# Performance work log

Measured on AMD Instinct MI355X. Metric: run time of the kernel, lower is better.

## Reference

```python
import jax, jax.numpy as jnp
import numpy as np

# dims
A, T, K, H, NH, F, L = 64, 50, 6, 128, 8, 60, 512
M = A * T * K          # 19200 mode nodes (layout: agent, time, mode)
AT = A * T             # 3200 agent-timestep nodes
NL = 10                # GA layers: t2m,l2m,m2m_h,m2m_a,m2m_s,t2n,l2n,n2n_h,n2n_a,n2n_s
FF = 4 * H
E = 150000


def _ln(x, g, b):
    mu = x.mean(-1, keepdims=True)
    var = jnp.mean((x - mu) ** 2, axis=-1, keepdims=True)
    return (x - mu) * jax.lax.rsqrt(var + 1e-5) * g + b


def _mlp(x, W1, b1, W2, b2):
    return jax.nn.relu(x @ W1 + b1) @ W2 + b2


def _edge_emb(attr, i, eW1, eb1, eW2, eb2):
    # pad raw edge features to width 5 so all embed MLPs share a stacked param layout
    x = jnp.pad(attr, ((0, 0), (0, 5 - attr.shape[-1])))
    return jax.nn.relu(x @ eW1[i] + eb1[i]) @ eW2[i] + eb2[i]


def _segment_softmax(scores, dst, n):
    smax = jax.ops.segment_max(scores, dst, num_segments=n)
    smax = jnp.where(jnp.isfinite(smax), smax, 0.0)
    ex = jnp.exp(scores - smax[dst])
    den = jax.ops.segment_sum(ex, dst, num_segments=n)
    return ex / (den[dst] + 1e-9)


def _graph_attention(i, x_src, x_dst, ei, edge_emb, p):
    (Wq, Wk, Wv, Wo, Wke, Wve, g1, b1, g2, b2, fW1, fb1, fW2, fb2) = p
    src, dst = ei[0], ei[1]
    dh = H // NH
    n_dst = x_dst.shape[0]
    xd = _ln(x_dst, g1[i], b1[i])
    xs = _ln(x_src, g1[i], b1[i])
    q = (xd @ Wq[i]).reshape(n_dst, NH, dh)
    k = (xs @ Wk[i])[src]            # gather per-edge keys  [E,H]
    v = (xs @ Wv[i])[src]
    if edge_emb is not None:
        k = k + edge_emb @ Wke[i]
        v = v + edge_emb @ Wve[i]
    k = k.reshape(-1, NH, dh)
    v = v.reshape(-1, NH, dh)
    scores = jnp.sum(q[dst] * k, axis=-1) / np.sqrt(dh)   # [E,NH]
    attn = _segment_softmax(scores, dst, n_dst)
    agg = jax.ops.segment_sum(attn[..., None] * v, dst, num_segments=n_dst)
    x = x_dst + agg.reshape(n_dst, H) @ Wo[i]
    h = _ln(x, g2[i], b2[i])
    return x + _mlp(h, fW1[i], fb1[i], fW2[i], fb2[i])


def _forward(a_input, l_embs, mode_tokens,
             emb_W1, emb_b1, emb_W2, emb_b2,
             ga_Wq, ga_Wk, ga_Wv, ga_Wo, ga_Wke, ga_Wve,
             ga_g1, ga_b1, ga_g2, ga_b2, ga_fW1, ga_fb1, ga_fW2, ga_fb2,
             tp_W1, tp_b1, tp_W2, tp_b2,
             pa_W1, pa_b1, pa_W2, pa_b2,
             tr_W1, tr_b1, tr_W2, tr_b2,
             t2m_attr, l2m_attr, m2m_h_attr, m2m_a_attr,
             t2m_ei, l2m_ei, m2m_h_ei, m2m_a_ei, m2m_s_ei):
    ga = (ga_Wq, ga_Wk, ga_Wv, ga_Wo, ga_Wke, ga_Wve,
          ga_g1, ga_b1, ga_g2, ga_b2, ga_fW1, ga_fb1, ga_fW2, ga_fb2)
    # agent embedding: TwoLayerMLP on [vel_len, vel_theta, length, width, type]
    a_embs = (jax.nn.relu(a_input @ emb_W1[0] + emb_b1[0]) @ emb_W2[0] + emb_b2[0]).reshape(AT, H)
    # mode tokens broadcast over (agent, time)
    m = jnp.broadcast_to(mode_tokens, (A, T, K, H)).reshape(M, H)
    # edge-attr embeddings (gather-compute pattern)
    t2m_e = _edge_emb(t2m_attr, 1, emb_W1, emb_b1, emb_W2, emb_b2)
    l2m_e = _edge_emb(l2m_attr, 2, emb_W1, emb_b1, emb_W2, emb_b2)
    m2m_h_e = _edge_emb(m2m_h_attr, 3, emb_W1, emb_b1, emb_W2, emb_b2)
    m2m_a_e = _edge_emb(m2m_a_attr, 4, emb_W1, emb_b1, emb_W2, emb_b2)
    # proposal stage
    m = _graph_attention(0, a_embs, m, t2m_ei, t2m_e, ga)
    m = _graph_attention(1, l_embs, m, l2m_ei, l2m_e, ga)
    m = _graph_attention(2, m, m, m2m_h_ei, m2m_h_e, ga)
    m = _graph_attention(3, m, m, m2m_a_ei, m2m_a_e, ga)
    m = _graph_attention(4, m, m, m2m_s_ei, None, ga)
    m_last = m.reshape(A, T, K, H)[:, -1]                 # [A,K,H]
    proposal = _mlp(m_last, tp_W1, tp_b1, tp_W2, tp_b2)   # [A,K,2F]
    anchor = _mlp(proposal, pa_W1, pa_b1, pa_W2, pa_b2)   # [A,K,H]
    # refinement stage on anchor-conditioned mode nodes
    n = (m.reshape(A, T, K, H) + anchor[:, None]).reshape(M, H)
    n = _graph_attention(5, a_embs, n, t2m_ei, t2m_e, ga)
    n = _graph_attention(6, l_embs, n, l2m_ei, l2m_e, ga)
    n = _graph_attention(7, n, n, m2m_h_ei, m2m_h_e, ga)
    n = _graph_attention(8, n, n, m2m_a_ei, m2m_a_e, ga)
    n = _graph_attention(9, n, n, m2m_s_ei, None, ga)
    n_last = n.reshape(A, T, K, H)[:, -1]
    refine = proposal + _mlp(n_last, tr_W1, tr_b1, tr_W2, tr_b2)
    return jnp.stack([proposal, refine])                  # [2,A,K,2F]


def setup_inputs() -> dict:
    key = jax.random.key(0)
    ks = list(jax.random.split(key, 64))
    it = iter(ks)
    nx = lambda: next(it)
    p = lambda *s: 0.02 * jax.random.normal(nx(), s, dtype=jnp.float32)
    inp = {}
    inp['a_input'] = jax.random.normal(nx(), (A, T, 5), dtype=jnp.float32)
    inp['l_embs'] = jax.random.normal(nx(), (L, H), dtype=jnp.float32)
    inp['mode_tokens'] = p(K, H)
    # stacked edge/feature embed MLPs: 0:a,1:t2m,2:l2m,3:m2m_h,4:m2m_a
    inp['emb_W1'] = p(5, 5, H); inp['emb_b1'] = jnp.zeros((5, H), jnp.float32)
    inp['emb_W2'] = p(5, H, H); inp['emb_b2'] = jnp.zeros((5, H), jnp.float32)
    # stacked GraphAttention params
    for nm in ['ga_Wq', 'ga_Wk', 'ga_Wv', 'ga_Wo', 'ga_Wke', 'ga_Wve']:
        inp[nm] = p(NL, H, H)
    inp['ga_g1'] = jnp.ones((NL, H), jnp.float32); inp['ga_b1'] = jnp.zeros((NL, H), jnp.float32)
    inp['ga_g2'] = jnp.ones((NL, H), jnp.float32); inp['ga_b2'] = jnp.zeros((NL, H), jnp.float32)
    inp['ga_fW1'] = p(NL, H, FF); inp['ga_fb1'] = jnp.zeros((NL, FF), jnp.float32)
    inp['ga_fW2'] = p(NL, FF, H); inp['ga_fb2'] = jnp.zeros((NL, H), jnp.float32)
    # heads
    inp['tp_W1'] = p(H, H); inp['tp_b1'] = jnp.zeros((H,), jnp.float32)
    inp['tp_W2'] = p(H, 2 * F); inp['tp_b2'] = jnp.zeros((2 * F,), jnp.float32)
    inp['pa_W1'] = p(2 * F, H); inp['pa_b1'] = jnp.zeros((H,), jnp.float32)
    inp['pa_W2'] = p(H, H); inp['pa_b2'] = jnp.zeros((H,), jnp.float32)
    inp['tr_W1'] = p(H, H); inp['tr_b1'] = jnp.zeros((H,), jnp.float32)
    inp['tr_W2'] = p(H, 2 * F); inp['tr_b2'] = jnp.zeros((2 * F,), jnp.float32)
    # raw edge features
    inp['t2m_attr'] = jax.random.normal(nx(), (E, 4), dtype=jnp.float32)
    inp['l2m_attr'] = jax.random.normal(nx(), (E, 3), dtype=jnp.float32)
    inp['m2m_h_attr'] = jax.random.normal(nx(), (E, 4), dtype=jnp.float32)
    inp['m2m_a_attr'] = jax.random.normal(nx(), (E, 3), dtype=jnp.float32)
    # edge indices (src row range differs per graph)
    ri = lambda hi: jax.random.randint(nx(), (E,), 0, hi, dtype=jnp.int32)
    inp['t2m_ei'] = jnp.stack([ri(AT), ri(M)])
    inp['l2m_ei'] = jnp.stack([ri(L), ri(M)])
    inp['m2m_h_ei'] = jnp.stack([ri(M), ri(M)])
    inp['m2m_a_ei'] = jnp.stack([ri(M), ri(M)])
    inp['m2m_s_ei'] = jnp.stack([ri(M), ri(M)])
    return inp


def reference(a_input, l_embs, mode_tokens,
              emb_W1, emb_b1, emb_W2, emb_b2,
              ga_Wq, ga_Wk, ga_Wv, ga_Wo, ga_Wke, ga_Wve,
              ga_g1, ga_b1, ga_g2, ga_b2, ga_fW1, ga_fb1, ga_fW2, ga_fb2,
              tp_W1, tp_b1, tp_W2, tp_b2,
              pa_W1, pa_b1, pa_W2, pa_b2,
              tr_W1, tr_b1, tr_W2, tr_b2,
              t2m_attr, l2m_attr, m2m_h_attr, m2m_a_attr,
              t2m_ei, l2m_ei, m2m_h_ei, m2m_a_ei, m2m_s_ei):
    return _forward(a_input, l_embs, mode_tokens,
                    emb_W1, emb_b1, emb_W2, emb_b2,
                    ga_Wq, ga_Wk, ga_Wv, ga_Wo, ga_Wke, ga_Wve,
                    ga_g1, ga_b1, ga_g2, ga_b2, ga_fW1, ga_fb1, ga_fW2, ga_fb2,
                    tp_W1, tp_b1, tp_W2, tp_b2,
                    pa_W1, pa_b1, pa_W2, pa_b2,
                    tr_W1, tr_b1, tr_W2, tr_b2,
                    t2m_attr, l2m_attr, m2m_h_attr, m2m_a_attr,
                    t2m_ei, l2m_ei, m2m_h_ei, m2m_a_ei, m2m_s_ei)
```

## Files before the change

### kernel.cpp

```cpp
#include <hip/hip_runtime.h>
#include <hip/hip_bf16.h>
#include <math.h>

#define DEV __device__ __forceinline__

typedef __attribute__((ext_vector_type(4))) float floatx4;
typedef __attribute__((ext_vector_type(8))) __bf16 bf16x8;

static constexpr int A_ = 64, T_ = 50, K_ = 6, H_ = 128, NH_ = 8, F_ = 60, L_ = 512;
static constexpr int M_  = A_ * T_ * K_;
static constexpr int AT_ = A_ * T_;
static constexpr int FF_ = 4 * H_;
static constexpr int NL_ = 10;
static constexpr int P2F = 2 * F_;
static constexpr int AK_ = A_ * K_;
static constexpr size_t WLAY = 196608;

DEV ushort f2bh(float f) {
    unsigned u = __float_as_uint(f);
    unsigned r = u + 0x7FFFu + ((u >> 16) & 1u);
    return (ushort)(r >> 16);
}
DEV float bh2f(ushort h) { return __uint_as_float(((unsigned)h) << 16); }

__global__ __launch_bounds__(256) void ln_kernel(const float* __restrict__ x,
                                                 const float* __restrict__ g,
                                                 const float* __restrict__ b,
                                                 float* __restrict__ y, int n) {
    int row = blockIdx.x * 4 + (threadIdx.x >> 6);
    int lane = threadIdx.x & 63;
    if (row >= n) return;
    const float* xr = x + (size_t)row * H_;
    float v0 = xr[lane], v1 = xr[lane + 64];
    float s = v0 + v1;
    for (int m = 32; m >= 1; m >>= 1) s += __shfl_xor(s, m, 64);
    float mu = s * (1.f / 128.f);
    float d0 = v0 - mu, d1 = v1 - mu;
    float vs = d0 * d0 + d1 * d1;
    for (int m = 32; m >= 1; m >>= 1) vs += __shfl_xor(vs, m, 64);
    float rs = rsqrtf(vs * (1.f / 128.f) + 1e-5f);
    float* yr = y + (size_t)row * H_;
    yr[lane]      = d0 * rs * g[lane] + b[lane];
    yr[lane + 64] = d1 * rs * g[lane + 64] + b[lane + 64];
}

template <int ACT, bool RES, bool OBF>
__global__ __launch_bounds__(256) void mgemm(const float* __restrict__ X,
                                             const ushort* __restrict__ Wh,
                                             const ushort* __restrict__ Wl,
                                             const float* __restrict__ bias,
                                             const float* __restrict__ res,
                                             float* __restrict__ Y,
                                             ushort* __restrict__ Yb,
                                             int n, int Kd, int C) {
    __shared__ ushort lds[4 * 8192];
    ushort* Xh  = lds;
    ushort* Xl  = lds + 8192;
    ushort* Wsh = lds + 16384;
    ushort* Wsl = lds + 24576;
    int row0 = blockIdx.x * 128, col0 = blockIdx.y * 128;
    int tid = threadIdx.x;
    int lane = tid & 63, wid = tid >> 6;
    int rbase = (wid >> 1) * 64, cbase = (wid & 1) * 64;
    int lrow = lane & 15, lk = lane >> 4;
    floatx4 acc[4][4];
#pragma unroll
    for (int a = 0; a < 4; a++)
#pragma unroll
        for (int b2 = 0; b2 < 4; b2++) acc[a][b2] = floatx4{0.f, 0.f, 0.f, 0.f};

    for (int k0 = 0; k0 < Kd; k0 += 64) {
#pragma unroll
        for (int i = 0; i < 8; i++) {
            int idx = tid + i * 256;
            int r = idx >> 4, kc = idx & 15;
            float4 v = *(const float4*)(X + (size_t)(row0 + r) * Kd + k0 + kc * 4);
            ushort h0 = f2bh(v.x), h1 = f2bh(v.y), h2 = f2bh(v.z), h3 = f2bh(v.w);
            ushort l0 = f2bh(v.x - bh2f(h0)), l1 = f2bh(v.y - bh2f(h1)),
                   l2 = f2bh(v.z - bh2f(h2)), l3 = f2bh(v.w - bh2f(h3));
            int base = (r << 6) + (((kc >> 1) ^ (r & 7)) << 3) + ((kc & 1) << 2);
            *(ushort4*)(Xh + base) = make_ushort4(h0, h1, h2, h3);
            *(ushort4*)(Xl + base) = make_ushort4(l0, l1, l2, l3);
        }
#pragma unroll
        for (int i = 0; i < 4; i++) {
            int idx = tid + i * 256;
            int c = idx >> 3, ch = idx & 7;
            int base = (c << 6) + ((ch ^ (c & 7)) << 3);
            size_t go = (size_t)(col0 + c) * Kd + k0 + ch * 8;
            *(float4*)(Wsh + base) = *(const float4*)(Wh + go);
            *(float4*)(Wsl + base) = *(const float4*)(Wl + go);
        }
        __syncthreads();
#pragma unroll
        for (int kk = 0; kk < 2; kk++) {
            int ch = kk * 4 + lk;
            bf16x8 xh[4], xl[4], wh[4], wl[4];
#pragma unroll
            for (int s = 0; s < 4; s++) {
                int r = rbase + s * 16 + lrow;
                int xoff = (r << 6) + ((ch ^ (r & 7)) << 3);
                xh[s] = *(const bf16x8*)(Xh + xoff);
                xl[s] = *(const bf16x8*)(Xl + xoff);
                int c = cbase + s * 16 + lrow;
                int woff = (c << 6) + ((ch ^ (c & 7)) << 3);
                wh[s] = *(const bf16x8*)(Wsh + woff);
                wl[s] = *(const bf16x8*)(Wsl + woff);
            }
#pragma unroll
            for (int sr = 0; sr < 4; sr++)
#pragma unroll
                for (int sc = 0; sc < 4; sc++) {
                    acc[sr][sc] = __builtin_amdgcn_mfma_f32_16x16x32_bf16(wh[sc], xh[sr], acc[sr][sc], 0, 0, 0);
                    acc[sr][sc] = __builtin_amdgcn_mfma_f32_16x16x32_bf16(wl[sc], xh[sr], acc[sr][sc], 0, 0, 0);
                    acc[sr][sc] = __builtin_amdgcn_mfma_f32_16x16x32_bf16(wh[sc], xl[sr], acc[sr][sc], 0, 0, 0);
                }
        }
        __syncthreads();
    }
#pragma unroll
    for (int sr = 0; sr < 4; sr++) {
        int row = row0 + rbase + sr * 16 + lrow;
#pragma unroll
        for (int sc = 0; sc < 4; sc++) {
            int col = col0 + cbase + sc * 16 + lk * 4;
            size_t o = (size_t)row * C + col;
            float4 v = make_float4(acc[sr][sc][0], acc[sr][sc][1],
                                   acc[sr][sc][2], acc[sr][sc][3]);
            if (bias) { float4 bv = *(const float4*)(bias + col);
                        v.x += bv.x; v.y += bv.y; v.z += bv.z; v.w += bv.w; }
            if (ACT == 1) { v.x = fmaxf(v.x, 0.f); v.y = fmaxf(v.y, 0.f);
                            v.z = fmaxf(v.z, 0.f); v.w = fmaxf(v.w, 0.f); }
            if (OBF) {
                *(ushort4*)(Yb + o) = make_ushort4(f2bh(v.x), f2bh(v.y), f2bh(v.z), f2bh(v.w));
            } else {
                if (RES) { float4 rv = *(const float4*)(res + o);
                           v.x += rv.x; v.y += rv.y; v.z += rv.z; v.w += rv.w; }
                *(float4*)(Y + o) = v;
            }
        }
    }
}

__global__ __launch_bounds__(256) void prep_w(const float* __restrict__ Wq,
                                              const float* __restrict__ Wk,
                                              const float* __restrict__ Wv,
                                              const float* __restrict__ Wo,
                                              const float* __restrict__ fW1,
                                              const float* __restrict__ fW2,
                                              ushort* __restrict__ oh,
                                              ushort* __restrict__ ol) {
    int l = blockIdx.y, t = blockIdx.x;
    const float* src; int K, C, tiles_c; size_t obase;
    if (t < 64) {
        int mi = t >> 4; t &= 15;
        src = (mi == 0 ? Wq : mi == 1 ? Wk : mi == 2 ? Wv : Wo) + (size_t)l * 16384;
        K = 128; C = 128; tiles_c = 4; obase = (size_t)l * WLAY + (size_t)mi * 16384;
    } else if (t < 128) {
        t -= 64; src = fW1 + (size_t)l * 65536;
        K = 128; C = 512; tiles_c = 16; obase = (size_t)l * WLAY + 65536;
    } else {
        t -= 128; src = fW2 + (size_t)l * 65536;
        K = 512; C = 128; tiles_c = 4; obase = (size_t)l * WLAY + 131072;
    }
    int tc = t % tiles_c, tk = t / tiles_c;
    __shared__ float tile[32][33];
    int tx = threadIdx.x & 31, ty = threadIdx.x >> 5;
#pragma unroll
    for (int i = 0; i < 4; i++) {
        int k = tk * 32 + ty + i * 8;
        tile[ty + i * 8][tx] = src[(size_t)k * C + tc * 32 + tx];
    }
    __syncthreads();
#pragma unroll
    for (int i = 0; i < 4; i++) {
        int c = tc * 32 + ty + i * 8;
        float v = tile[tx][ty + i * 8];
        ushort h = f2bh(v);
        ushort lo = f2bh(v - bh2f(h));
        size_t o = obase + (size_t)c * K + tk * 32 + tx;
        oh[o] = h; ol[o] = lo;
    }
}

template <int ACT, bool RES>
__global__ void small_gemm(const float* __restrict__ X, const float* __restrict__ W,
                           const float* __restrict__ bias, const float* __restrict__ res,
                           float* __restrict__ Y, int n, int Kd, int C) {
    int idx = blockIdx.x * 256 + threadIdx.x;
    if (idx >= n * C) return;
    int row = idx / C, c = idx - row * C;
    float a = bias ? bias[c] : 0.f;
    const float* xr = X + (size_t)row * Kd;
    for (int k = 0; k < Kd; k++) a = fmaf(xr[k], W[(size_t)k * C + c], a);
    if (ACT == 1) a = fmaxf(a, 0.f);
    if (RES) a += res[idx];
    Y[idx] = a;
}

__global__ __launch_bounds__(256) void combine_fast(const float* __restrict__ eW2,
                                                    const float* __restrict__ Wke,
                                                    const float* __restrict__ Wve,
                                                    float* __restrict__ cW) {
    __shared__ float Xs[128 * 36];
    __shared__ float Ws[32 * 128];
    int x = blockIdx.x;
    int li = x & 7, kv = x >> 3;
    int l = li < 4 ? li : li + 1;
    int g = (li & 3) + 1;
    const float* E2 = eW2 + (size_t)g * 16384;
    const float* Wp = (kv ? Wve : Wke) + (size_t)l * 16384;
    float* out = cW + (size_t)l * 32768 + kv * 128;
    int tid = threadIdx.x;
    int tc = tid & 15, tr = tid >> 4;
    int cA = tc * 4, rA = tr * 4;
    float acc[8][8] = {};
    for (int j0 = 0; j0 < 128; j0 += 32) {
#pragma unroll
        for (int i = 0; i < 4; i++) {
            int idx = tid + i * 256;
            int r = idx >> 3, jc = idx & 7;
            *(float4*)(Xs + r * 36 + jc * 4) =
                *(const float4*)(E2 + (size_t)r * 128 + j0 + jc * 4);
        }
#pragma unroll
        for (int i = 0; i < 4; i++) {
            int idx = tid + i * 256;
            int cc = idx & 31, jj = idx >> 5;
            *(float4*)(Ws + jj * 128 + cc * 4) =
                *(const float4*)(Wp + (size_t)(j0 + jj) * 128 + cc * 4);
        }
        __syncthreads();
#pragma unroll 8
        for (int jj = 0; jj < 32; jj++) {
            float4 w0 = *(const float4*)(Ws + jj * 128 + cA);
            float4 w1 = *(const float4*)(Ws + jj * 128 + cA + 64);
            float xr[8];
#pragma unroll
            for (int i2 = 0; i2 < 4; i2++) {
                xr[i2]     = Xs[(rA + i2) * 36 + jj];
                xr[4 + i2] = Xs[(rA + i2 + 64) * 36 + jj];
            }
#pragma unroll
            for (int i2 = 0; i2 < 8; i2++) {
                float xv = xr[i2];
                acc[i2][0] = fmaf(xv, w0.x, acc[i2][0]);
                acc[i2][1] = fmaf(xv, w0.y, acc[i2][1]);
                acc[i2][2] = fmaf(xv, w0.z, acc[i2][2]);
                acc[i2][3] = fmaf(xv, w0.w, acc[i2][3]);
                acc[i2][4] = fmaf(xv, w1.x, acc[i2][4]);
                acc[i2][5] = fmaf(xv, w1.y, acc[i2][5]);
                acc[i2][6] = fmaf(xv, w1.z, acc[i2][6]);
                acc[i2][7] = fmaf(xv, w1.w, acc[i2][7]);
            }
        }
        __syncthreads();
    }
#pragma unroll
    for (int i = 0; i < 8; i++) {
        int r = (i < 4) ? (rA + i) : (rA + i + 60);
#pragma unroll
        for (int chh = 0; chh < 2; chh++) {
            int c = cA + chh * 64;
            *(float4*)(out + (size_t)r * 256 + c) =
                make_float4(acc[i][chh * 4 + 0], acc[i][chh * 4 + 1],
                            acc[i][chh * 4 + 2], acc[i][chh * 4 + 3]);
        }
    }
}
__global__ void combine_bias(const float* __restrict__ eb2,
                             const float* __restrict__ Wke,
                             const float* __restrict__ Wve,
                             float* __restrict__ cb) {
    int x = blockIdx.x;
    int li = x & 7, kv = x >> 3;
    int l = li < 4 ? li : li + 1;
    int g = (li & 3) + 1;
    const float* Wp = (kv ? Wve : Wke) + (size_t)l * 16384;
    const float* eb = eb2 + g * 128;
    int cc = threadIdx.x;
    float a = 0.f;
    for (int j = 0; j < 128; j++) a = fmaf(eb[j], Wp[(size_t)j * 128 + cc], a);
    cb[l * 256 + kv * 128 + cc] = a;
}

__global__ void zero_i32(int* __restrict__ p, int n) {
    int i = blockIdx.x * 256 + threadIdx.x;
    if (i < n) p[i] = 0;
}
__global__ void hist_kernel(const int* __restrict__ dst, int E, int* __restrict__ deg) {
    int e = blockIdx.x * 256 + threadIdx.x;
    if (e < E) atomicAdd(&deg[dst[e]], 1);
}
__global__ __launch_bounds__(256) void exscan5(const int* __restrict__ deg0,
                                               int* __restrict__ off0,
                                               int* __restrict__ cursor0, int n) {
    int g = blockIdx.x;
    const int* deg = deg0 + (size_t)g * n;
    int* off = off0 + (size_t)g * (n + 1);
    int* cursor = cursor0 + (size_t)g * n;
    __shared__ int wsum[4];
    __shared__ int carry;
    int tid = threadIdx.x, lane = tid & 63, w = tid >> 6;
    if (tid == 0) carry = 0;
    __syncthreads();
    for (int base = 0; base < n; base += 256) {
        int v = (base + tid < n) ? deg[base + tid] : 0;
        int incl = v;
        for (int d = 1; d < 64; d <<= 1) {
            int t = __shfl_up(incl, d, 64);
            if (lane >= d) incl += t;
        }
        if (lane == 63) wsum[w] = incl;
        __syncthreads();
        int woff = 0;
        for (int i = 0; i < w; i++) woff += wsum[i];
        int total = wsum[0] + wsum[1] + wsum[2] + wsum[3];
        int excl = carry + woff + incl - v;
        if (base + tid < n) { off[base + tid] = excl; cursor[base + tid] = excl; }
        __syncthreads();
        if (tid == 0) carry += total;
        __syncthreads();
    }
    if (threadIdx.x == 0) off[n] = carry;
}
__global__ void scatter_kernel(const int* __restrict__ dst, int E,
                               int* __restrict__ cursor, int* __restrict__ eids) {
    int e = blockIdx.x * 256 + threadIdx.x;
    if (e < E) { int p = atomicAdd(&cursor[dst[e]], 1); eids[p] = e; }
}
__global__ void sort_edges(const int* __restrict__ eid, const int* __restrict__ srcArr,
                           const float* __restrict__ attr, int aw, int E,
                           int* __restrict__ esrc, float4* __restrict__ eattr) {
    int pos = blockIdx.x * 256 + threadIdx.x;
    if (pos >= E) return;
    int e = eid[pos];
    esrc[pos] = srcArr[e];
    if (attr) {
        float4 v;
        v.x = attr[(size_t)e * aw + 0];
        v.y = attr[(size_t)e * aw + 1];
        v.z = (aw > 2) ? attr[(size_t)e * aw + 2] : 0.f;
        v.w = (aw > 3) ? attr[(size_t)e * aw + 3] : 0.f;
        eattr[pos] = v;
    }
}

__global__ __launch_bounds__(256) void prep_g(const float* __restrict__ q,
                                              const float* __restrict__ cWl,
                                              const float* __restrict__ cbl,
                                              ushort* __restrict__ g,
                                              float* __restrict__ sb) {
    __shared__ float qs[8 * 132];
    int tid = threadIdx.x;
    int cp = tid & 127, hb = (tid >> 7) * 4;
    float ck[64];
    {
        const float* csrc = cWl + (size_t)cp * 256 + hb * 16;
#pragma unroll
        for (int t4 = 0; t4 < 16; t4++) {
            float4 v = *(const float4*)(csrc + t4 * 4);
            ck[t4 * 4 + 0] = v.x; ck[t4 * 4 + 1] = v.y;
            ck[t4 * 4 + 2] = v.z; ck[t4 * 4 + 3] = v.w;
        }
    }
    int d0 = blockIdx.x * 8;
    {
        int dl = tid >> 5, col = (tid & 31) * 4;
        *(float4*)(qs + dl * 132 + col) = *(const float4*)(q + (size_t)(d0 + dl) * 128 + col);
    }
    __syncthreads();
#pragma unroll
    for (int dl = 0; dl < 8; dl++) {
        const float* qr = qs + dl * 132 + hb * 16;
        float a0 = 0.f, a1 = 0.f, a2 = 0.f, a3 = 0.f;
#pragma unroll
        for (int t = 0; t < 16; t++) {
            a0 = fmaf(ck[t],      qr[t],      a0);
            a1 = fmaf(ck[16 + t], qr[16 + t], a1);
            a2 = fmaf(ck[32 + t], qr[32 + t], a2);
            a3 = fmaf(ck[48 + t], qr[48 + t], a3);
        }
        ushort4 o = make_ushort4(f2bh(a0 * 0.25f), f2bh(a1 * 0.25f),
                                 f2bh(a2 * 0.25f), f2bh(a3 * 0.25f));
        *(ushort4*)(g + (size_t)(d0 + dl) * 1024 + cp * 8 + hb) = o;
    }
    if (tid < 64) {
        int dl = tid >> 3, h = tid & 7;
        const float* qr = qs + dl * 132 + h * 16;
        const float* cbr = cbl + h * 16;
        float a = 0.f;
#pragma unroll
        for (int t = 0; t < 16; t++) a = fmaf(cbr[t], qr[t], a);
        sb[(d0 + dl) * 8 + h] = a * 0.25f;
    }
}

__global__ __launch_bounds__(256) void attn_fact(const int* __restrict__ off,
                                                 const int* __restrict__ esrc,
                                                 const float4* __restrict__ eattr,
                                                 const ushort* __restrict__ g,
                                                 const float* __restrict__ sb,
                                                 const float* __restrict__ eW1,
                                                 const float* __restrict__ eb1,
                                                 const float* __restrict__ q,
                                                 const ushort* __restrict__ kvp,
                                                 ushort* __restrict__ hsum,
                                                 float* __restrict__ vxacc,
                                                 float* __restrict__ den) {
    __shared__ float lds[4 * 144];
    int w = threadIdx.x >> 6, l = threadIdx.x & 63;
    int i = l & 15, hlo = l >> 4;
    float* hw = lds + w * 144;
    int d = blockIdx.x * 4 + w;
    int beg = off[d], end = off[d + 1];
    float q0 = q[(size_t)d * 128 + l] * 0.25f;
    float q1 = q[(size_t)d * 128 + 64 + l] * 0.25f;
    float gA[8], gB[8];
#pragma unroll
    for (int j = 0; j < 8; j++) {
        gA[j] = bh2f(g[(size_t)d * 1024 + (j * 16 + i) * 8 + hlo]);
        gB[j] = bh2f(g[(size_t)d * 1024 + (j * 16 + i) * 8 + hlo + 4]);
    }
    float sbA = sb[d * 8 + hlo], sbB = sb[d * 8 + 4 + hlo];
    float w1a[4], w1b[4];
#pragma unroll
    for (int j = 0; j < 4; j++) { w1a[j] = eW1[j * 128 + l]; w1b[j] = eW1[j * 128 + 64 + l]; }
    float ebA = eb1[l], ebB = eb1[64 + l];
    float dnA = 0.f, dnB = 0.f;
    float accL[8] = {}, accH[8] = {};
    float va0 = 0.f, va1 = 0.f;
    float4 atA = make_float4(0.f, 0.f, 0.f, 0.f), atB = atA;
    ushort kA0 = 0, kA1 = 0, vA0 = 0, vA1 = 0;
    ushort kB0 = 0, kB1 = 0, vB0 = 0, vB1 = 0;
    auto LOADE = [&](int p, float4& at, ushort& ka, ushort& kb, ushort& va, ushort& vb) {
        int s = esrc[p]; at = eattr[p];
        const ushort* r = kvp + (size_t)s * 256;
        ka = r[l]; kb = r[64 + l];
        va = r[128 + l]; vb = r[192 + l];
    };
    if (beg < end) LOADE(beg, atA, kA0, kA1, vA0, vA1);
    if (beg + 1 < end) LOADE(beg + 1, atB, kB0, kB1, vB0, vB1);
    for (int pos = beg; pos < end; pos++) {
        float4 at = atA;
        ushort rk0 = kA0, rk1 = kA1, rv0 = vA0, rv1 = vA1;
        atA = atB; kA0 = kB0; kA1 = kB1; vA0 = vB0; vA1 = vB1;
        if (pos + 2 < end) LOADE(pos + 2, atB, kB0, kB1, vB0, vB1);
        float h0 = fmaxf(ebA + at.x * w1a[0] + at.y * w1a[1] + at.z * w1a[2] + at.w * w1a[3], 0.f);
        float h1 = fmaxf(ebB + at.x * w1b[0] + at.y * w1b[1] + at.z * w1b[2] + at.w * w1b[3], 0.f);
        hw[l] = h0; hw[64 + l] = h1;
        __builtin_amdgcn_wave_barrier();
        float pA = q0 * bh2f(rk0), pB = q1 * bh2f(rk1);
#pragma unroll
        for (int j = 0; j < 8; j++) {
            float hv = hw[j * 16 + i];
            pA = fmaf(hv, gA[j], pA);
            pB = fmaf(hv, gB[j], pB);
        }
#pragma unroll
        for (int msk = 1; msk < 16; msk <<= 1) {
            pA += __shfl_xor(pA, msk, 64);
            pB += __shfl_xor(pB, msk, 64);
        }
        float wA = __expf(pA + sbA);
        float wB = __expf(pB + sbB);
        dnA += wA; dnB += wB;
        va0 = fmaf(wA, bh2f(rv0), va0);
        va1 = fmaf(wB, bh2f(rv1), va1);
        if (i == 0) { hw[128 + hlo] = wA; hw[132 + hlo] = wB; }
        __builtin_amdgcn_wave_barrier();
        float4 WA = *(float4*)(hw + 128), WB = *(float4*)(hw + 132);
#pragma unroll
        for (int j = 0; j < 4; j++) {
            float wa = ((const float*)&WA)[j];
            float wb = ((const float*)&WB)[j];
            accL[j]     = fmaf(wa, h0, accL[j]);
            accH[j]     = fmaf(wa, h1, accH[j]);
            accL[4 + j] = fmaf(wb, h0, accL[4 + j]);
            accH[4 + j] = fmaf(wb, h1, accH[4 + j]);
        }
    }
#pragma unroll
    for (int h = 0; h < 8; h++) {
        hsum[(size_t)d * 1024 + h * 128 + l]      = f2bh(accL[h]);
        hsum[(size_t)d * 1024 + h * 128 + 64 + l] = f2bh(accH[h]);
    }
    vxacc[(size_t)d * 128 + l] = va0;
    vxacc[(size_t)d * 128 + 64 + l] = va1;
    if (i == 0) { den[d * 8 + hlo] = dnA; den[d * 8 + 4 + hlo] = dnB; }
}

__global__ __launch_bounds__(256) void attn_plain(const int* __restrict__ off,
                                                  const int* __restrict__ esrc,
                                                  const float* __restrict__ q,
                                                  const ushort* __restrict__ kvp,
                                                  float* __restrict__ agg) {
    int lane = threadIdx.x & 63;
    int d = blockIdx.x * 4 + (threadIdx.x >> 6);
    int beg = off[d], end = off[d + 1];
    float q0 = q[(size_t)d * 128 + lane] * 0.25f;
    float q1 = q[(size_t)d * 128 + 64 + lane] * 0.25f;
    float den0 = 0.f, den1 = 0.f, acc0 = 0.f, acc1 = 0.f;
    ushort kA0 = 0, kA1 = 0, vA0 = 0, vA1 = 0;
    ushort kB0 = 0, kB1 = 0, vB0 = 0, vB1 = 0;
    auto LOADE = [&](int p, ushort& ka, ushort& kb, ushort& va, ushort& vb) {
        int s = esrc[p];
        const ushort* r = kvp + (size_t)s * 256;
        ka = r[lane]; kb = r[64 + lane];
        va = r[128 + lane]; vb = r[192 + lane];
    };
    if (beg < end) LOADE(beg, kA0, kA1, vA0, vA1);
    if (beg + 1 < end) LOADE(beg + 1, kB0, kB1, vB0, vB1);
    for (int pos = beg; pos < end; pos++) {
        ushort rk0 = kA0, rk1 = kA1, rv0 = vA0, rv1 = vA1;
        kA0 = kB0; kA1 = kB1; vA0 = vB0; vA1 = vB1;
        if (pos + 2 < end) LOADE(pos + 2, kB0, kB1, vB0, vB1);
        float p0 = q0 * bh2f(rk0), p1 = q1 * bh2f(rk1);
#pragma unroll
        for (int msk = 1; msk < 16; msk <<= 1) {
            p0 += __shfl_xor(p0, msk, 64);
            p1 += __shfl_xor(p1, msk, 64);
        }
        float w0 = __expf(p0), w1 = __expf(p1);
        den0 += w0; den1 += w1;
        acc0 = fmaf(w0, bh2f(rv0), acc0);
        acc1 = fmaf(w1, bh2f(rv1), acc1);
    }
    agg[(size_t)d * 128 + lane]      = acc0 / (den0 + 1e-9f);
    agg[(size_t)d * 128 + 64 + lane] = acc1 / (den1 + 1e-9f);
}

static constexpr int HST_ = 1092;
__global__ __launch_bounds__(256) void agg_fin(const ushort* __restrict__ hsum,
                                               const float* __restrict__ vxacc,
                                               const float* __restrict__ den,
                                               const float* __restrict__ cWl,
                                               const float* __restrict__ cbl,
                                               float* __restrict__ agg) {
    __shared__ float Cvs[128 * 128];
    __shared__ float hstage[8 * HST_];
    __shared__ float dens[64];
    int tid = threadIdx.x;
    {
        int cp = tid >> 1, cb0 = (tid & 1) * 64;
#pragma unroll
        for (int kq = 0; kq < 16; kq++)
            *(float4*)(Cvs + cp * 128 + cb0 + kq * 4) =
                *(const float4*)(cWl + (size_t)cp * 256 + 128 + cb0 + kq * 4);
    }
    int j = tid & 31, dsel = tid >> 5;
    int c4 = j * 4, h = j >> 2;
    float4 cvb = *(const float4*)(cbl + 128 + c4);
    for (int d0 = blockIdx.x * 8; d0 < M_; d0 += gridDim.x * 8) {
        __syncthreads();
        int r = tid * 4;
#pragma unroll
        for (int k = 0; k < 8; k++) {
            ushort4 u = *(const ushort4*)(hsum + (size_t)(d0 + k) * 1024 + r);
            *(float4*)(hstage + k * HST_ + (r >> 7) * 136 + (r & 127)) =
                make_float4(bh2f(u.x), bh2f(u.y), bh2f(u.z), bh2f(u.w));
        }
        if (tid < 64) dens[tid] = den[d0 * 8 + tid];
        __syncthreads();
        int d = d0 + dsel;
        float dn = dens[dsel * 8 + h];
        float inv = 1.f / (dn + 1e-9f);
        float cf = dn * inv;
        float a0 = 0.f, a1 = 0.f, a2 = 0.f, a3 = 0.f;
        const float* hrow = hstage + dsel * HST_ + h * 136;
#pragma unroll 4
        for (int cpp = 0; cpp < 128; cpp++) {
            float hs = hrow[cpp];
            float4 cv = *(float4*)(Cvs + cpp * 128 + c4);
            a0 = fmaf(hs, cv.x, a0); a1 = fmaf(hs, cv.y, a1);
            a2 = fmaf(hs, cv.z, a2); a3 = fmaf(hs, cv.w, a3);
        }
        float4 vv = *(const float4*)(vxacc + (size_t)d * 128 + c4);
        float4 o;
        o.x = (vv.x + a0) * inv + cvb.x * cf;
        o.y = (vv.y + a1) * inv + cvb.y * cf;
        o.z = (vv.z + a2) * inv + cvb.z * cf;
        o.w = (vv.w + a3) * inv + cvb.w * cf;
        *(float4*)(agg + (size_t)d * 128 + c4) = o;
    }
}

__global__ void mode_init(float* __restrict__ m, const float* __restrict__ mt) {
    int idx = blockIdx.x * 256 + threadIdx.x;
    if (idx >= M_ * H_) return;
    int node = idx >> 7, c = idx & 127;
    m[idx] = mt[(node % K_) * H_ + c];
}
__global__ void extract_last(const float* __restrict__ m, float* __restrict__ out) {
    int idx = blockIdx.x * 256 + threadIdx.x;
    if (idx >= AK_ * H_) return;
    int row = idx >> 7, c = idx & 127;
    int a = row / K_, k = row - a * K_;
    int node = (a * T_ + (T_ - 1)) * K_ + k;
    out[idx] = m[(size_t)node * H_ + c];
}
__global__ void add_anchor(float* __restrict__ m, const float* __restrict__ anchor) {
    int idx = blockIdx.x * 256 + threadIdx.x;
    if (idx >= M_ * H_) return;
    int node = idx >> 7, c = idx & 127;
    int a = node / (T_ * K_), k = node % K_;
    m[idx] += anchor[(size_t)(a * K_ + k) * H_ + c];
}

extern "C" void kernel_launch(void* const* d_in, const int* in_sizes, int n_in,
                              void* d_out, int out_size, void* d_ws, size_t ws_size,
                              hipStream_t stream) {
    const float* a_input     = (const float*)d_in[0];
    const float* l_embs      = (const float*)d_in[1];
    const float* mode_tokens = (const float*)d_in[2];
    const float* emb_W1 = (const float*)d_in[3];
    const float* emb_b1 = (const float*)d_in[4];
    const float* emb_W2 = (const float*)d_in[5];
    const float* emb_b2 = (const float*)d_in[6];
    const float* ga_Wq  = (const float*)d_in[7];
    const float* ga_Wk  = (const float*)d_in[8];
    const float* ga_Wv  = (const float*)d_in[9];
    const float* ga_Wo  = (const float*)d_in[10];
    const float* ga_Wke = (const float*)d_in[11];
    const float* ga_Wve = (const float*)d_in[12];
    const float* ga_g1  = (const float*)d_in[13];
    const float* ga_b1  = (const float*)d_in[14];
    const float* ga_g2  = (const float*)d_in[15];
    const float* ga_b2  = (const float*)d_in[16];
    const float* ga_fW1 = (const float*)d_in[17];
    const float* ga_fb1 = (const float*)d_in[18];
    const float* ga_fW2 = (const float*)d_in[19];
    const float* ga_fb2 = (const float*)d_in[20];
    const float* tp_W1 = (const float*)d_in[21];
    const float* tp_b1 = (const float*)d_in[22];
    const float* tp_W2 = (const float*)d_in[23];
    const float* tp_b2 = (const float*)d_in[24];
    const float* pa_W1 = (const float*)d_in[25];
    const float* pa_b1 = (const float*)d_in[26];
    const float* pa_W2 = (const float*)d_in[27];
    const float* pa_b2 = (const float*)d_in[28];
    const float* tr_W1 = (const float*)d_in[29];
    const float* tr_b1 = (const float*)d_in[30];
    const float* tr_W2 = (const float*)d_in[31];
    const float* tr_b2 = (const float*)d_in[32];
    const float* attrs[4] = { (const float*)d_in[33], (const float*)d_in[34],
                              (const float*)d_in[35], (const float*)d_in[36] };
    const int* eis[5] = { (const int*)d_in[37], (const int*)d_in[38], (const int*)d_in[39],
                          (const int*)d_in[40], (const int*)d_in[41] };
    int Es[5];
    int Emax = 0;
    for (int i = 0; i < 5; i++) { Es[i] = in_sizes[37 + i] / 2; if (Es[i] > Emax) Emax = Es[i]; }

    size_t off = 0;
    auto alloc = [&](size_t nbytes) -> char* {
        char* p = (char*)d_ws + off;
        off += ((nbytes + 255) / 256) * 256;
        return p;
    };
    float* cW     = (float*)alloc((size_t)NL_ * 128 * 256 * 4);
    float* cb     = (float*)alloc((size_t)NL_ * 256 * 4);
    ushort* wbh   = (ushort*)alloc((size_t)NL_ * WLAY * 2);
    ushort* wbl   = (ushort*)alloc((size_t)NL_ * WLAY * 2);
    float* a_embs = (float*)alloc((size_t)AT_ * H_ * 4);
    float* m      = (float*)alloc((size_t)M_ * H_ * 4);
    float* xd_ln  = (float*)alloc((size_t)M_ * H_ * 4);
    float* xs_ln  = (float*)alloc((size_t)AT_ * H_ * 4);
    float* q      = (float*)alloc((size_t)M_ * H_ * 4);
    ushort* kvb   = (ushort*)alloc((size_t)M_ * 256 * 2);
    float* agg    = (float*)alloc((size_t)M_ * H_ * 4);
    float* big    = (float*)alloc((size_t)M_ * FF_ * 4);
    ushort* gbuf  = (ushort*)alloc((size_t)M_ * 1024 * 2);
    ushort* hsumb = (ushort*)alloc((size_t)M_ * 1024 * 2);
    float* vxacc  = (float*)alloc((size_t)M_ * H_ * 4);
    float* den    = (float*)alloc((size_t)M_ * 8 * 4);
    float* sb     = (float*)alloc((size_t)M_ * 8 * 4);
    int* csr_off  = (int*)alloc((size_t)5 * (M_ + 1) * 4);
    int* csr_eid  = (int*)alloc((size_t)5 * Emax * 4);
    int* esrc     = (int*)alloc((size_t)5 * Emax * 4);
    float4* eattr = (float4*)alloc((size_t)4 * Emax * 16);
    int* deg5     = (int*)alloc((size_t)5 * M_ * 4);
    int* cursor5  = (int*)alloc((size_t)5 * M_ * 4);
    float* mlast  = (float*)alloc((size_t)AK_ * H_ * 4);
    float* hbuf   = (float*)alloc((size_t)AK_ * H_ * 4);
    float* anchor = (float*)alloc((size_t)AK_ * H_ * 4);
    (void)ws_size; (void)n_in;

    float* outp = (float*)d_out;

    zero_i32<<<(5 * M_ + 255) / 256, 256, 0, stream>>>(deg5, 5 * M_);
    for (int gI = 0; gI < 5; gI++)
        hist_kernel<<<(Es[gI] + 255) / 256, 256, 0, stream>>>(eis[gI] + Es[gI], Es[gI], deg5 + (size_t)gI * M_);
    exscan5<<<5, 256, 0, stream>>>(deg5, csr_off, cursor5, M_);
    for (int gI = 0; gI < 5; gI++)
        scatter_kernel<<<(Es[gI] + 255) / 256, 256, 0, stream>>>(eis[gI] + Es[gI], Es[gI],
            cursor5 + (size_t)gI * M_, csr_eid + (size_t)gI * Emax);
    for (int gI = 0; gI < 5; gI++) {
        int aw = (gI == 0 || gI == 2) ? 4 : (gI == 4 ? 0 : 3);
        sort_edges<<<(Es[gI] + 255) / 256, 256, 0, stream>>>(
            csr_eid + (size_t)gI * Emax, eis[gI], (gI < 4) ? attrs[gI] : nullptr, aw, Es[gI],
            esrc + (size_t)gI * Emax, eattr + (size_t)gI * Emax);
    }

    prep_w<<<dim3(192, 10), 256, 0, stream>>>(ga_Wq, ga_Wk, ga_Wv, ga_Wo, ga_fW1, ga_fW2, wbh, wbl);
    combine_fast<<<16, 256, 0, stream>>>(emb_W2, ga_Wke, ga_Wve, cW);
    combine_bias<<<16, 128, 0, stream>>>(emb_b2, ga_Wke, ga_Wve, cb);

    small_gemm<1, false><<<(AT_ * H_ + 255) / 256, 256, 0, stream>>>(a_input, emb_W1, emb_b1, nullptr, big, AT_, 5, H_);
    small_gemm<0, false><<<(AT_ * H_ + 255) / 256, 256, 0, stream>>>(big, emb_W2, emb_b2, nullptr, a_embs, AT_, H_, H_);
    mode_init<<<(M_ * H_ + 255) / 256, 256, 0, stream>>>(m, mode_tokens);

    struct Cfg { const float* srcX; int n_src; int gi; bool hasE; };
    Cfg cfgs[10] = {
        { a_embs, AT_, 0, true }, { l_embs, L_, 1, true },
        { nullptr, M_, 2, true }, { nullptr, M_, 3, true },
        { nullptr, M_, 4, false },
        { a_embs, AT_, 0, true }, { l_embs, L_, 1, true },
        { nullptr, M_, 2, true }, { nullptr, M_, 3, true },
        { nullptr, M_, 4, false },
    };

    for (int l = 0; l < 10; l++) {
        const Cfg& cf = cfgs[l];
        const int* offg = csr_off + cf.gi * (M_ + 1);
        const int* esrcg = esrc + (size_t)cf.gi * Emax;
        const float4* eattrg = eattr + (size_t)cf.gi * Emax;
        const float* g1 = ga_g1 + l * H_; const float* b1 = ga_b1 + l * H_;
        size_t wb = (size_t)l * WLAY;

        ln_kernel<<<M_ / 4, 256, 0, stream>>>(m, g1, b1, xd_ln, M_);
        mgemm<0, false, false><<<dim3(M_ / 128, 1), 256, 0, stream>>>(
            xd_ln, wbh + wb, wbl + wb, nullptr, nullptr, q, nullptr, M_, 128, 128);
        const float* kvsrc = xd_ln;
        int nkv = M_;
        if (cf.srcX) {
            ln_kernel<<<cf.n_src / 4, 256, 0, stream>>>(cf.srcX, g1, b1, xs_ln, cf.n_src);
            kvsrc = xs_ln; nkv = cf.n_src;
        }
        mgemm<0, false, true><<<dim3(nkv / 128, 2), 256, 0, stream>>>(
            kvsrc, wbh + wb + 16384, wbl + wb + 16384, nullptr, nullptr, nullptr, kvb, nkv, 128, 256);

        if (cf.hasE) {
            int gg = (l < 5) ? l + 1 : l - 4;
            const float* eW1g = emb_W1 + (size_t)gg * 5 * H_;
            const float* eb1g = emb_b1 + (size_t)gg * H_;
            prep_g<<<M_ / 8, 256, 0, stream>>>(q, cW + (size_t)l * 128 * 256, cb + l * 256, gbuf, sb);
            attn_fact<<<M_ / 4, 256, 0, stream>>>(offg, esrcg, eattrg, gbuf, sb, eW1g, eb1g,
                                                  q, kvb, hsumb, vxacc, den);
            agg_fin<<<256, 256, 0, stream>>>(hsumb, vxacc, den,
                                             cW + (size_t)l * 128 * 256, cb + l * 256, agg);
        } else {
            attn_plain<<<M_ / 4, 256, 0, stream>>>(offg, esrcg, q, kvb, agg);
        }

        mgemm<0, true, false><<<dim3(M_ / 128, 1), 256, 0, stream>>>(
            agg, wbh + wb + 49152, wbl + wb + 49152, nullptr, m, m, nullptr, M_, 128, 128);
        ln_kernel<<<M_ / 4, 256, 0, stream>>>(m, ga_g2 + l * H_, ga_b2 + l * H_, xd_ln, M_);
        mgemm<1, false, false><<<dim3(M_ / 128, 4), 256, 0, stream>>>(
            xd_ln, wbh + wb + 65536, wbl + wb + 65536, ga_fb1 + l * FF_, nullptr, big, nullptr, M_, 128, 512);
        mgemm<0, true, false><<<dim3(M_ / 128, 1), 256, 0, stream>>>(
            big, wbh + wb + 131072, wbl + wb + 131072, ga_fb2 + l * H_, m, m, nullptr, M_, 512, 128);

        if (l == 4) {
            extract_last<<<(AK_ * H_ + 255) / 256, 256, 0, stream>>>(m, mlast);
            small_gemm<1, false><<<(AK_ * H_ + 255) / 256, 256, 0, stream>>>(mlast, tp_W1, tp_b1, nullptr, hbuf, AK_, H_, H_);
            small_gemm<0, false><<<(AK_ * P2F + 255) / 256, 256, 0, stream>>>(hbuf, tp_W2, tp_b2, nullptr, outp, AK_, H_, P2F);
            small_gemm<1, false><<<(AK_ * H_ + 255) / 256, 256, 0, stream>>>(outp, pa_W1, pa_b1, nullptr, hbuf, AK_, P2F, H_);
            small_gemm<0, false><<<(AK_ * H_ + 255) / 256, 256, 0, stream>>>(hbuf, pa_W2, pa_b2, nullptr, anchor, AK_, H_, H_);
            add_anchor<<<(M_ * H_ + 255) / 256, 256, 0, stream>>>(m, anchor);
        }
    }

    extract_last<<<(AK_ * H_ + 255) / 256, 256, 0, stream>>>(m, mlast);
    small_gemm<1, false><<<(AK_ * H_ + 255) / 256, 256, 0, stream>>>(mlast, tr_W1, tr_b1, nullptr, hbuf, AK_, H_, H_);
    small_gemm<0, true><<<(AK_ * P2F + 255) / 256, 256, 0, stream>>>(hbuf, tr_W2, tr_b2, outp, outp + AK_ * P2F, AK_, H_, P2F);
}
```

Baseline: 2.632 ms.

## Fuse LayerNorm into GEMM loads, merge Q/KV GEMMs, degree-sort attention rows

Result: slower. 3.314 ms (+25.9%).

```diff
diff --git a/kernel.cpp b/kernel.cpp
--- a/kernel.cpp
+++ b/kernel.cpp
@@ -23,10 +23,9 @@
 }
 DEV float bh2f(ushort h) { return __uint_as_float(((unsigned)h) << 16); }
 
-__global__ __launch_bounds__(256) void ln_kernel(const float* __restrict__ x,
-                                                 const float* __restrict__ g,
-                                                 const float* __restrict__ b,
-                                                 float* __restrict__ y, int n) {
+__global__ __launch_bounds__(256) void ln_stats(const float* __restrict__ x,
+                                                float* __restrict__ mu,
+                                                float* __restrict__ rs, int n) {
     int row = blockIdx.x * 4 + (threadIdx.x >> 6);
     int lane = threadIdx.x & 63;
     if (row >= n) return;
@@ -34,17 +33,17 @@
     float v0 = xr[lane], v1 = xr[lane + 64];
     float s = v0 + v1;
     for (int m = 32; m >= 1; m >>= 1) s += __shfl_xor(s, m, 64);
-    float mu = s * (1.f / 128.f);
-    float d0 = v0 - mu, d1 = v1 - mu;
+    float m_ = s * (1.f / 128.f);
+    float d0 = v0 - m_, d1 = v1 - m_;
     float vs = d0 * d0 + d1 * d1;
     for (int m = 32; m >= 1; m >>= 1) vs += __shfl_xor(vs, m, 64);
-    float rs = rsqrtf(vs * (1.f / 128.f) + 1e-5f);
-    float* yr = y + (size_t)row * H_;
-    yr[lane]      = d0 * rs * g[lane] + b[lane];
-    yr[lane + 64] = d1 * rs * g[lane + 64] + b[lane + 64];
-}
-
-template <int ACT, bool RES, bool OBF>
+    if (lane == 0) {
+        mu[row] = m_;
+        rs[row] = rsqrtf(vs * (1.f / 128.f) + 1e-5f);
+    }
+}
+
+template <int ACT, bool RES, int OMODE, bool LNX>
 __global__ __launch_bounds__(256) void mgemm(const float* __restrict__ X,
                                              const ushort* __restrict__ Wh,
                                              const ushort* __restrict__ Wl,
@@ -52,6 +51,10 @@
                                              const float* __restrict__ res,
                                              float* __restrict__ Y,
                                              ushort* __restrict__ Yb,
+                                             const float* __restrict__ muv,
+                                             const float* __restrict__ rsv,
+                                             const float* __restrict__ lng,
+                                             const float* __restrict__ lnb,
                                              int n, int Kd, int C) {
     __shared__ ushort lds[4 * 8192];
     ushort* Xh  = lds;
@@ -70,11 +73,25 @@
         for (int b2 = 0; b2 < 4; b2++) acc[a][b2] = floatx4{0.f, 0.f, 0.f, 0.f};
 
     for (int k0 = 0; k0 < Kd; k0 += 64) {
+        float4 g4, b4;
+        if (LNX) {
+            int kcol = k0 + (tid & 15) * 4;
+            g4 = *(const float4*)(lng + kcol);
+            b4 = *(const float4*)(lnb + kcol);
+        }
 #pragma unroll
         for (int i = 0; i < 8; i++) {
             int idx = tid + i * 256;
             int r = idx >> 4, kc = idx & 15;
             float4 v = *(const float4*)(X + (size_t)(row0 + r) * Kd + k0 + kc * 4);
+            if (LNX) {
+                float mur = muv[row0 + r];
+                float rsr = rsv[row0 + r];
+                v.x = (v.x - mur) * rsr * g4.x + b4.x;
+                v.y = (v.y - mur) * rsr * g4.y + b4.y;
+                v.z = (v.z - mur) * rsr * g4.z + b4.z;
+                v.w = (v.w - mur) * rsr * g4.w + b4.w;
+            }
             ushort h0 = f2bh(v.x), h1 = f2bh(v.y), h2 = f2bh(v.z), h3 = f2bh(v.w);
             ushort l0 = f2bh(v.x - bh2f(h0)), l1 = f2bh(v.y - bh2f(h1)),
                    l2 = f2bh(v.z - bh2f(h2)), l3 = f2bh(v.w - bh2f(h3));
@@ -124,19 +141,27 @@
 #pragma unroll
         for (int sc = 0; sc < 4; sc++) {
             int col = col0 + cbase + sc * 16 + lk * 4;
-            size_t o = (size_t)row * C + col;
             float4 v = make_float4(acc[sr][sc][0], acc[sr][sc][1],
                                    acc[sr][sc][2], acc[sr][sc][3]);
             if (bias) { float4 bv = *(const float4*)(bias + col);
                         v.x += bv.x; v.y += bv.y; v.z += bv.z; v.w += bv.w; }
             if (ACT == 1) { v.x = fmaxf(v.x, 0.f); v.y = fmaxf(v.y, 0.f);
                             v.z = fmaxf(v.z, 0.f); v.w = fmaxf(v.w, 0.f); }
-            if (OBF) {
-                *(ushort4*)(Yb + o) = make_ushort4(f2bh(v.x), f2bh(v.y), f2bh(v.z), f2bh(v.w));
-            } else {
+            if (OMODE == 0) {
+                size_t o = (size_t)row * C + col;
                 if (RES) { float4 rv = *(const float4*)(res + o);
                            v.x += rv.x; v.y += rv.y; v.z += rv.z; v.w += rv.w; }
                 *(float4*)(Y + o) = v;
+            } else if (OMODE == 1) {
+                size_t o = (size_t)row * C + col;
+                *(ushort4*)(Yb + o) = make_ushort4(f2bh(v.x), f2bh(v.y), f2bh(v.z), f2bh(v.w));
+            } else {
+                if (col0 == 0) {
+                    *(float4*)(Y + (size_t)row * 128 + col) = v;
+                } else {
+                    *(ushort4*)(Yb + (size_t)row * 256 + (col - 128)) =
+                        make_ushort4(f2bh(v.x), f2bh(v.y), f2bh(v.z), f2bh(v.w));
+                }
             }
         }
     }
@@ -346,6 +371,26 @@
     }
 }
 
+__global__ void hist_deg(const int* __restrict__ deg, int n, int* __restrict__ dh) {
+    int d = blockIdx.x * 256 + threadIdx.x;
+    if (d < n) { int b = deg[d]; if (b > 32) b = 32; atomicAdd(&dh[b], 1); }
+}
+__global__ void exscan33(int* __restrict__ dh0, int* __restrict__ dcur0) {
+    int g = blockIdx.x;
+    int* h = dh0 + g * 33;
+    int* c = dcur0 + g * 33;
+    if (threadIdx.x == 0) {
+        int acc = 0;
+        for (int i = 0; i < 33; i++) { int v = h[i]; h[i] = acc; c[i] = acc; acc += v; }
+    }
+}
+__global__ void scatter_ord(const int* __restrict__ deg, int n,
+                            int* __restrict__ dcur, int* __restrict__ dord) {
+    int d = blockIdx.x * 256 + threadIdx.x;
+    if (d < n) { int b = deg[d]; if (b > 32) b = 32;
+                 int p = atomicAdd(&dcur[b], 1); dord[p] = d; }
+}
+
 __global__ __launch_bounds__(256) void prep_g(const float* __restrict__ q,
                                               const float* __restrict__ cWl,
                                               const float* __restrict__ cbl,
@@ -396,7 +441,8 @@
     }
 }
 
-__global__ __launch_bounds__(256) void attn_fact(const int* __restrict__ off,
+__global__ __launch_bounds__(256) void attn_fact(const int* __restrict__ dord,
+                                                 const int* __restrict__ off,
                                                  const int* __restrict__ esrc,
                                                  const float4* __restrict__ eattr,
                                                  const ushort* __restrict__ g,
@@ -412,7 +458,7 @@
     int w = threadIdx.x >> 6, l = threadIdx.x & 63;
     int i = l & 15, hlo = l >> 4;
     float* hw = lds + w * 144;
-    int d = blockIdx.x * 4 + w;
+    int d = dord[blockIdx.x * 4 + w];
     int beg = off[d], end = off[d + 1];
     float q0 = q[(size_t)d * 128 + l] * 0.25f;
     float q1 = q[(size_t)d * 128 + 64 + l] * 0.25f;
@@ -490,13 +536,14 @@
     if (i == 0) { den[d * 8 + hlo] = dnA; den[d * 8 + 4 + hlo] = dnB; }
 }
 
-__global__ __launch_bounds__(256) void attn_plain(const int* __restrict__ off,
+__global__ __launch_bounds__(256) void attn_plain(const int* __restrict__ dord,
+                                                  const int* __restrict__ off,
                                                   const int* __restrict__ esrc,
                                                   const float* __restrict__ q,
                                                   const ushort* __restrict__ kvp,
                                                   float* __restrict__ agg) {
     int lane = threadIdx.x & 63;
-    int d = blockIdx.x * 4 + (threadIdx.x >> 6);
+    int d = dord[blockIdx.x * 4 + (threadIdx.x >> 6)];
     int beg = off[d], end = off[d + 1];
     float q0 = q[(size_t)d * 128 + lane] * 0.25f;
     float q1 = q[(size_t)d * 128 + 64 + lane] * 0.25f;
@@ -663,8 +710,6 @@
     ushort* wbl   = (ushort*)alloc((size_t)NL_ * WLAY * 2);
     float* a_embs = (float*)alloc((size_t)AT_ * H_ * 4);
     float* m      = (float*)alloc((size_t)M_ * H_ * 4);
-    float* xd_ln  = (float*)alloc((size_t)M_ * H_ * 4);
-    float* xs_ln  = (float*)alloc((size_t)AT_ * H_ * 4);
     float* q      = (float*)alloc((size_t)M_ * H_ * 4);
     ushort* kvb   = (ushort*)alloc((size_t)M_ * 256 * 2);
     float* agg    = (float*)alloc((size_t)M_ * H_ * 4);
@@ -674,12 +719,21 @@
     float* vxacc  = (float*)alloc((size_t)M_ * H_ * 4);
     float* den    = (float*)alloc((size_t)M_ * 8 * 4);
     float* sb     = (float*)alloc((size_t)M_ * 8 * 4);
+    float* muM    = (float*)alloc((size_t)M_ * 4);
+    float* rsM    = (float*)alloc((size_t)M_ * 4);
+    float* muA    = (float*)alloc((size_t)AT_ * 4);
+    float* rsA    = (float*)alloc((size_t)AT_ * 4);
+    float* muL    = (float*)alloc((size_t)L_ * 4);
+    float* rsL    = (float*)alloc((size_t)L_ * 4);
     int* csr_off  = (int*)alloc((size_t)5 * (M_ + 1) * 4);
     int* csr_eid  = (int*)alloc((size_t)5 * Emax * 4);
     int* esrc     = (int*)alloc((size_t)5 * Emax * 4);
     float4* eattr = (float4*)alloc((size_t)4 * Emax * 16);
     int* deg5     = (int*)alloc((size_t)5 * M_ * 4);
     int* cursor5  = (int*)alloc((size_t)5 * M_ * 4);
+    int* dord5    = (int*)alloc((size_t)5 * M_ * 4);
+    int* dh5      = (int*)alloc((size_t)5 * 33 * 4);
+    int* dcur5    = (int*)alloc((size_t)5 * 33 * 4);
     float* mlast  = (float*)alloc((size_t)AK_ * H_ * 4);
     float* hbuf   = (float*)alloc((size_t)AK_ * H_ * 4);
     float* anchor = (float*)alloc((size_t)AK_ * H_ * 4);
@@ -688,6 +742,7 @@
     float* outp = (float*)d_out;
 
     zero_i32<<<(5 * M_ + 255) / 256, 256, 0, stream>>>(deg5, 5 * M_);
+    zero_i32<<<1, 256, 0, stream>>>(dh5, 5 * 33);
     for (int gI = 0; gI < 5; gI++)
         hist_kernel<<<(Es[gI] + 255) / 256, 256, 0, stream>>>(eis[gI] + Es[gI], Es[gI], deg5 + (size_t)gI * M_);
     exscan5<<<5, 256, 0, stream>>>(deg5, csr_off, cursor5, M_);
@@ -700,6 +755,12 @@
             csr_eid + (size_t)gI * Emax, eis[gI], (gI < 4) ? attrs[gI] : nullptr, aw, Es[gI],
             esrc + (size_t)gI * Emax, eattr + (size_t)gI * Emax);
     }
+    for (int gI = 0; gI < 5; gI++)
+        hist_deg<<<(M_ + 255) / 256, 256, 0, stream>>>(deg5 + (size_t)gI * M_, M_, dh5 + gI * 33);
+    exscan33<<<5, 64, 0, stream>>>(dh5, dcur5);
+    for (int gI = 0; gI < 5; gI++)
+        scatter_ord<<<(M_ + 255) / 256, 256, 0, stream>>>(deg5 + (size_t)gI * M_, M_,
+            dcur5 + gI * 33, dord5 + (size_t)gI * M_);
 
     prep_w<<<dim3(192, 10), 256, 0, stream>>>(ga_Wq, ga_Wk, ga_Wv, ga_Wo, ga_fW1, ga_fW2, wbh, wbl);
     combine_fast<<<16, 256, 0, stream>>>(emb_W2, ga_Wke, ga_Wve, cW);
@@ -708,15 +769,17 @@
     small_gemm<1, false><<<(AT_ * H_ + 255) / 256, 256, 0, stream>>>(a_input, emb_W1, emb_b1, nullptr, big, AT_, 5, H_);
     small_gemm<0, false><<<(AT_ * H_ + 255) / 256, 256, 0, stream>>>(big, emb_W2, emb_b2, nullptr, a_embs, AT_, H_, H_);
     mode_init<<<(M_ * H_ + 255) / 256, 256, 0, stream>>>(m, mode_tokens);
-
-    struct Cfg { const float* srcX; int n_src; int gi; bool hasE; };
+    ln_stats<<<AT_ / 4, 256, 0, stream>>>(a_embs, muA, rsA, AT_);
+    ln_stats<<<L_ / 4, 256, 0, stream>>>(l_embs, muL, rsL, L_);
+
+    struct Cfg { const float* srcX; const float* muS; const float* rsS; int n_src; int gi; bool hasE; };
     Cfg cfgs[10] = {
-        { a_embs, AT_, 0, true }, { l_embs, L_, 1, true },
-        { nullptr, M_, 2, true }, { nullptr, M_, 3, true },
-        { nullptr, M_, 4, false },
-        { a_embs, AT_, 0, true }, { l_embs, L_, 1, true },
-        { nullptr, M_, 2, true }, { nullptr, M_, 3, true },
-        { nullptr, M_, 4, false },
+        { a_embs, muA, rsA, AT_, 0, true }, { l_embs, muL, rsL, L_, 1, true },
+        { nullptr, nullptr, nullptr, M_, 2, true }, { nullptr, nullptr, nullptr, M_, 3, true },
+        { nullptr, nullptr, nullptr, M_, 4, false },
+        { a_embs, muA, rsA, AT_, 0, true }, { l_embs, muL, rsL, L_, 1, true },
+        { nullptr, nullptr, nullptr, M_, 2, true }, { nullptr, nullptr, nullptr, M_, 3, true },
+        { nullptr, nullptr, nullptr, M_, 4, false },
     };
 
     for (int l = 0; l < 10; l++) {
@@ -724,41 +787,47 @@
         const int* offg = csr_off + cf.gi * (M_ + 1);
         const int* esrcg = esrc + (size_t)cf.gi * Emax;
         const float4* eattrg = eattr + (size_t)cf.gi * Emax;
+        const int* dordg = dord5 + (size_t)cf.gi * M_;
         const float* g1 = ga_g1 + l * H_; const float* b1 = ga_b1 + l * H_;
         size_t wb = (size_t)l * WLAY;
 
-        ln_kernel<<<M_ / 4, 256, 0, stream>>>(m, g1, b1, xd_ln, M_);
-        mgemm<0, false, false><<<dim3(M_ / 128, 1), 256, 0, stream>>>(
-            xd_ln, wbh + wb, wbl + wb, nullptr, nullptr, q, nullptr, M_, 128, 128);
-        const float* kvsrc = xd_ln;
-        int nkv = M_;
+        ln_stats<<<M_ / 4, 256, 0, stream>>>(m, muM, rsM, M_);
         if (cf.srcX) {
-            ln_kernel<<<cf.n_src / 4, 256, 0, stream>>>(cf.srcX, g1, b1, xs_ln, cf.n_src);
-            kvsrc = xs_ln; nkv = cf.n_src;
-        }
-        mgemm<0, false, true><<<dim3(nkv / 128, 2), 256, 0, stream>>>(
-            kvsrc, wbh + wb + 16384, wbl + wb + 16384, nullptr, nullptr, nullptr, kvb, nkv, 128, 256);
+            mgemm<0, false, 0, true><<<dim3(M_ / 128, 1), 256, 0, stream>>>(
+                m, wbh + wb, wbl + wb, nullptr, nullptr, q, nullptr,
+                muM, rsM, g1, b1, M_, 128, 128);
+            mgemm<0, false, 1, true><<<dim3(cf.n_src / 128, 2), 256, 0, stream>>>(
+                cf.srcX, wbh + wb + 16384, wbl + wb + 16384, nullptr, nullptr, nullptr, kvb,
+                cf.muS, cf.rsS, g1, b1, cf.n_src, 128, 256);
+        } else {
+            mgemm<0, false, 2, true><<<dim3(M_ / 128, 3), 256, 0, stream>>>(
+                m, wbh + wb, wbl + wb, nullptr, nullptr, q, kvb,
+                muM, rsM, g1, b1, M_, 128, 384);
+        }
 
         if (cf.hasE) {
             int gg = (l < 5) ? l + 1 : l - 4;
             const float* eW1g = emb_W1 + (size_t)gg * 5 * H_;
             const float* eb1g = emb_b1 + (size_t)gg * H_;
             prep_g<<<M_ / 8, 256, 0, stream>>>(q, cW + (size_t)l * 128 * 256, cb + l * 256, gbuf, sb);
-            attn_fact<<<M_ / 4, 256, 0, stream>>>(offg, esrcg, eattrg, gbuf, sb, eW1g, eb1g,
+            attn_fact<<<M_ / 4, 256, 0, stream>>>(dordg, offg, esrcg, eattrg, gbuf, sb, eW1g, eb1g,
                                                   q, kvb, hsumb, vxacc, den);
             agg_fin<<<256, 256, 0, stream>>>(hsumb, vxacc, den,
                                              cW + (size_t)l * 128 * 256, cb + l * 256, agg);
         } else {
-            attn_plain<<<M_ / 4, 256, 0, stream>>>(offg, esrcg, q, kvb, agg);
-        }
-
-        mgemm<0, true, false><<<dim3(M_ / 128, 1), 256, 0, stream>>>(
-            agg, wbh + wb + 49152, wbl + wb + 49152, nullptr, m, m, nullptr, M_, 128, 128);
-        ln_kernel<<<M_ / 4, 256, 0, stream>>>(m, ga_g2 + l * H_, ga_b2 + l * H_, xd_ln, M_);
-        mgemm<1, false, false><<<dim3(M_ / 128, 4), 256, 0, stream>>>(
-            xd_ln, wbh + wb + 65536, wbl + wb + 65536, ga_fb1 + l * FF_, nullptr, big, nullptr, M_, 128, 512);
-        mgemm<0, true, false><<<dim3(M_ / 128, 1), 256, 0, stream>>>(
-            big, wbh + wb + 131072, wbl + wb + 131072, ga_fb2 + l * H_, m, m, nullptr, M_, 512, 128);
+            attn_plain<<<M_ / 4, 256, 0, stream>>>(dordg, offg, esrcg, q, kvb, agg);
+        }
+
+        mgemm<0, true, 0, false><<<dim3(M_ / 128, 1), 256, 0, stream>>>(
+            agg, wbh + wb + 49152, wbl + wb + 49152, nullptr, m, m, nullptr,
+            nullptr, nullptr, nullptr, nullptr, M_, 128, 128);
+        ln_stats<<<M_ / 4, 256, 0, stream>>>(m, muM, rsM, M_);
+        mgemm<1, false, 0, true><<<dim3(M_ / 128, 4), 256, 0, stream>>>(
+            m, wbh + wb + 65536, wbl + wb + 65536, ga_fb1 + l * FF_, nullptr, big, nullptr,
+            muM, rsM, ga_g2 + l * H_, ga_b2 + l * H_, M_, 128, 512);
+        mgemm<0, true, 0, false><<<dim3(M_ / 128, 1), 256, 0, stream>>>(
+            big, wbh + wb + 131072, wbl + wb + 131072, ga_fb2 + l * H_, m, m, nullptr,
+            nullptr, nullptr, nullptr, nullptr, M_, 512, 128);
 
         if (l == 4) {
             extract_last<<<(AK_ * H_ + 255) / 256, 256, 0, stream>>>(m, mlast);
```
